# Kernel tuning notes

Hardware: AMD Instinct MI355X
Metric: run time of the kernel (lower is better)

Reference implementation:

```python
import jax, jax.numpy as jnp
from jax import lax
import numpy as np

B, N, C, HEADS = 8, 4096, 512, 16
HD = C // HEADS


def rope2d(x, h, w, base=10000.0):
    # x: [b, h, w, c]; 2D axial RoPE as in the torch `rope` helper
    c = x.shape[-1]
    k_max = c // 4  # feature_dim // (2 * len(channel_dims))
    theta = 1.0 / (base ** (jnp.arange(k_max, dtype=jnp.float32) / k_max))  # [k_max]
    ii = jnp.arange(h, dtype=jnp.float32)[:, None, None]  # row index
    jj = jnp.arange(w, dtype=jnp.float32)[None, :, None]  # col index
    ang = jnp.concatenate([
        jnp.broadcast_to(ii * theta, (h, w, k_max)),
        jnp.broadcast_to(jj * theta, (h, w, k_max)),
    ], axis=-1)  # [h, w, c//2]
    cos, sin = jnp.cos(ang), jnp.sin(ang)
    xp = x.reshape(x.shape[0], h, w, c // 2, 2)
    xr, xi = xp[..., 0], xp[..., 1]
    out = jnp.stack([xr * cos - xi * sin, xi * cos + xr * sin], axis=-1)
    return out.reshape(x.shape)


def setup_inputs() -> dict:
    key = jax.random.key(0)
    k1, k2, k3, k4, k5 = jax.random.split(key, 5)
    x = jax.random.normal(k1, (B, N, C), dtype=jnp.float32)
    Wqk = jax.random.normal(k2, (C, 2 * C), dtype=jnp.float32) * 0.02
    bqk = jax.random.normal(k3, (2 * C,), dtype=jnp.float32) * 0.02
    lepe_w = jax.random.normal(k4, (C, 1, 3, 3), dtype=jnp.float32) * 0.05  # depthwise OIHW
    lepe_b = jax.random.normal(k5, (C,), dtype=jnp.float32) * 0.02
    return {"x": x, "h": 64, "w": 64, "Wqk": Wqk, "bqk": bqk, "lepe_w": lepe_w, "lepe_b": lepe_b}


def reference(x, h, w, Wqk, bqk, lepe_w, lepe_b):
    b, n, c = x.shape
    hd = c // HEADS
    qk = x @ Wqk + bqk                       # [b, n, 2c]
    q = jax.nn.elu(qk[..., :c]) + 1.0        # ELU+1 feature map
    k = jax.nn.elu(qk[..., c:]) + 1.0
    v = x
    q_rope = rope2d(q.reshape(b, h, w, c), h, w).reshape(b, n, HEADS, hd)
    k_rope = rope2d(k.reshape(b, h, w, c), h, w).reshape(b, n, HEADS, hd)
    qh = q.reshape(b, n, HEADS, hd)
    kh = k.reshape(b, n, HEADS, hd)
    vh = v.reshape(b, n, HEADS, hd)
    k_mean = kh.mean(axis=1)                 # [b, HEADS, hd]
    z = 1.0 / (jnp.einsum('bnhd,bhd->bnh', qh, k_mean) + 1e-6)  # [b, n, HEADS]
    inv_n = 1.0 / jnp.float32(n)
    kv = jnp.einsum('bnhd,bnhe->bhde', k_rope, vh) * inv_n       # [b, HEADS, hd, hd]
    attn = jnp.einsum('bnhd,bhde->bnhe', q_rope, kv) * z[..., None]
    out = attn.reshape(b, n, c)
    # depthwise 3x3 LePE on v (== x) as NCHW image
    v_img = x.reshape(b, h, w, c).transpose(0, 3, 1, 2)
    lepe = lax.conv_general_dilated(v_img, lepe_w, (1, 1), 'SAME',
                                    feature_group_count=c,
                                    dimension_numbers=('NCHW', 'OIHW', 'NCHW'))
    lepe = lepe + lepe_b[None, :, None, None]
    out = out + lepe.transpose(0, 2, 3, 1).reshape(b, n, c)
    return out
```

## Files before the change

### kernel.cpp

```cpp
#include <hip/hip_runtime.h>
#include <stdint.h>

static constexpr int BATCH = 8;
static constexpr int NTOK  = 4096;
static constexpr int CDIM  = 512;
static constexpr int NCOL  = 1024;
static constexpr int MROWS = BATCH * NTOK;
static constexpr int KDIM  = 512;

static constexpr size_t OFF_KSUM = 0;
static constexpr size_t OFF_KV   = 16384;
static constexpr size_t OFF_XB   = 540672;
static constexpr size_t OFF_WT   = OFF_XB + 33554432;
static constexpr size_t OFF_QP   = OFF_WT + 1048576;
static constexpr size_t OFF_KR   = OFF_QP + 33554432;
static constexpr size_t OFF_TRIG = OFF_KR + 33554432;
static constexpr size_t OFF_WT9  = OFF_TRIG + 65536;
static constexpr size_t WS_NEED  = OFF_WT9 + 18432;

static constexpr int KV_CHUNKS = 64;
static constexpr int KV_OUT    = BATCH * 16 * 32 * 32;

typedef __attribute__((ext_vector_type(8))) short bf16x8;
typedef __attribute__((ext_vector_type(4))) float f32x4;
typedef __attribute__((ext_vector_type(8))) unsigned short u16x8;

__device__ __forceinline__ float bf2f(unsigned short u) {
  union { unsigned int i; float f; } v; v.i = ((unsigned int)u) << 16; return v.f;
}
__device__ __forceinline__ unsigned short f2bf(float f) {
  union { float f; unsigned int i; } v; v.f = f;
  unsigned int b = v.i + 0x7FFFu + ((v.i >> 16) & 1u);
  return (unsigned short)(b >> 16);
}
__device__ __forceinline__ void gload16(const void* g, void* l) {
  __builtin_amdgcn_global_load_lds(
      (const __attribute__((address_space(1))) unsigned int*)g,
      (__attribute__((address_space(3))) unsigned int*)l,
      16, 0, 0);
}
__device__ __forceinline__ float elu1(float v) {
  return v > 0.f ? v + 1.f : __expf(v);
}

__global__ void prep_kernel(const float* __restrict__ x, const float* __restrict__ Wqk,
                            const float* __restrict__ lepe_w,
                            float* __restrict__ wsf, unsigned short* __restrict__ xb,
                            unsigned short* __restrict__ wT, float2* __restrict__ trig,
                            float* __restrict__ wt9) {
  const int ZN = (int)(OFF_XB / 4);
  const int XN = MROWS * CDIM / 8;
  const int WN = (KDIM * NCOL) / 8;
  const int TN = 64 * 128;
  const int W9 = 9 * 512;
  const int total = ZN + XN + WN + TN + W9;
  for (int i = blockIdx.x * blockDim.x + threadIdx.x; i < total;
       i += gridDim.x * blockDim.x) {
    if (i < ZN) {
      wsf[i] = 0.f;
    } else if (i < ZN + XN) {
      const int j = i - ZN;
      const float4* xp = (const float4*)x + (size_t)j * 2;
      const float4 a = xp[0], b4 = xp[1];
      u16x8 o;
      o[0] = f2bf(a.x);  o[1] = f2bf(a.y);  o[2] = f2bf(a.z);  o[3] = f2bf(a.w);
      o[4] = f2bf(b4.x); o[5] = f2bf(b4.y); o[6] = f2bf(b4.z); o[7] = f2bf(b4.w);
      *((u16x8*)xb + j) = o;
    } else if (i < ZN + XN + WN) {
      const int j = i - ZN - XN;
      const int nc8 = j & 127;
      const int k   = j >> 7;
      const float4* wp = (const float4*)(Wqk + (size_t)k * NCOL + nc8 * 8);
      const float4 a = wp[0], b4 = wp[1];
      const float vals[8] = {a.x, a.y, a.z, a.w, b4.x, b4.y, b4.z, b4.w};
      const int nc0 = nc8 * 8;
#pragma unroll
      for (int t = 0; t < 8; ++t) wT[(size_t)(nc0 + t) * KDIM + k] = f2bf(vals[t]);
    } else if (i < ZN + XN + WN + TN) {
      const int j = i - ZN - XN - WN;
      const int tt = j & 127;
      const int pos = j >> 7;
      const float theta = __expf(-(float)tt * 0.07195578415f);
      const float ang = (float)pos * theta;
      float s, c;
      sincosf(ang, &s, &c);
      trig[pos * 128 + tt] = make_float2(c, s);
    } else {
      const int j = i - ZN - XN - WN - TN;
      const int tap = j >> 9;
      const int c   = j & 511;
      wt9[tap * 512 + c] = lepe_w[c * 9 + tap];
    }
  }
}

__global__ __launch_bounds__(512)
void gemm_kernel(const unsigned short* __restrict__ xb, const unsigned short* __restrict__ wT,
                 const float* __restrict__ bqk, const float2* __restrict__ trig,
                 unsigned short* __restrict__ qp, unsigned short* __restrict__ kr,
                 float* __restrict__ ksum) {
  __shared__ __align__(16) unsigned short S[3][2][8192];
  float* Cst = (float*)&S[0][0][0];
  const int tid = threadIdx.x;
  const int wid = tid >> 6;
  const int l = tid & 63;
  const int la = l & 15, lg = l >> 4;
  const int wm = wid >> 2, wn = wid & 3;
  const int nt = blockIdx.x;
  const int m0 = blockIdx.y * 256;
  const int n0 = nt * 256;

  f32x4 acc[8][4];
#pragma unroll
  for (int i = 0; i < 8; ++i)
#pragma unroll
    for (int j = 0; j < 4; ++j) acc[i][j] = (f32x4){0.f, 0.f, 0.f, 0.f};

  const int srow = tid >> 2;
  const int scol = ((tid & 3) ^ ((tid >> 3) & 3)) * 8;
  const int rsw = (la >> 1) & 3;
  const int rslot = (lg ^ rsw) * 8;

#define STG_A(kt, bb, rr) gload16(xb + (size_t)(m0 + (rr) * 128 + srow) * KDIM + (kt) * 32 + scol, \
                                  &S[bb][0][(rr) * 4096 + tid * 8])
#define STG_B(kt, bb, rr) gload16(wT + (size_t)(n0 + (rr) * 128 + srow) * KDIM + (kt) * 32 + scol, \
                                  &S[bb][1][(rr) * 4096 + tid * 8])

  STG_A(0, 0, 0); STG_A(0, 0, 1); STG_B(0, 0, 0); STG_B(0, 0, 1);
  STG_A(1, 1, 0); STG_A(1, 1, 1); STG_B(1, 1, 0); STG_B(1, 1, 1);
  asm volatile("s_waitcnt vmcnt(4)" ::: "memory");
  __builtin_amdgcn_s_barrier();
  __builtin_amdgcn_sched_barrier(0);

  for (int kt = 0; kt < 16; ++kt) {
    const int cur = kt % 3;
    const int nx2 = (kt + 2) % 3;
    bf16x8 af[4], bf[4];
#pragma unroll
    for (int i = 0; i < 4; ++i)
      af[i] = *(const bf16x8*)&S[cur][0][(wm * 128 + i * 16 + la) * 32 + rslot];
#pragma unroll
    for (int j = 0; j < 4; ++j)
      bf[j] = *(const bf16x8*)&S[cur][1][(wn * 64 + j * 16 + la) * 32 + rslot];
    if (kt + 2 < 16) { STG_A(kt + 2, nx2, 0); STG_A(kt + 2, nx2, 1); }
    __builtin_amdgcn_s_barrier();
    asm volatile("s_waitcnt lgkmcnt(0)" ::: "memory");
    __builtin_amdgcn_sched_barrier(0);
    __builtin_amdgcn_s_setprio(1);
#pragma unroll
    for (int i = 0; i < 4; ++i)
#pragma unroll
      for (int j = 0; j < 4; ++j)
        acc[i][j] = __builtin_amdgcn_mfma_f32_16x16x32_bf16(af[i], bf[j], acc[i][j], 0, 0, 0);
    __builtin_amdgcn_s_setprio(0);
    __builtin_amdgcn_s_barrier();
#pragma unroll
    for (int i = 0; i < 4; ++i)
      af[i] = *(const bf16x8*)&S[cur][0][(wm * 128 + (4 + i) * 16 + la) * 32 + rslot];
    if (kt + 2 < 16) { STG_B(kt + 2, nx2, 0); STG_B(kt + 2, nx2, 1); }
    __builtin_amdgcn_s_barrier();
    asm volatile("s_waitcnt lgkmcnt(0)" ::: "memory");
    __builtin_amdgcn_sched_barrier(0);
    __builtin_amdgcn_s_setprio(1);
#pragma unroll
    for (int i = 0; i < 4; ++i)
#pragma unroll
      for (int j = 0; j < 4; ++j)
        acc[4 + i][j] = __builtin_amdgcn_mfma_f32_16x16x32_bf16(af[i], bf[j], acc[4 + i][j], 0, 0, 0);
    __builtin_amdgcn_s_setprio(0);
    if (kt < 14) {
      asm volatile("s_waitcnt vmcnt(4)" ::: "memory");
    } else if (kt == 14) {
      asm volatile("s_waitcnt vmcnt(0)" ::: "memory");
    }
    __builtin_amdgcn_s_barrier();
    __builtin_amdgcn_sched_barrier(0);
  }
#undef STG_A
#undef STG_B

  const bool isq = (nt < 2);
  const int bidx = m0 >> 12;
  float colsum[4] = {0.f, 0.f, 0.f, 0.f};
#pragma unroll
  for (int j = 0; j < 4; ++j) {
    const float bias = bqk[n0 + wn * 64 + j * 16 + la];
#pragma unroll
    for (int i = 0; i < 8; ++i) {
#pragma unroll
      for (int r = 0; r < 4; ++r) {
        const float v = elu1(acc[i][j][r] + bias);
        acc[i][j][r] = v;
        if (!isq) colsum[j] += v;
      }
    }
  }
  if (!isq) {
#pragma unroll
    for (int j = 0; j < 4; ++j) {
      float s = colsum[j];
      s += __shfl_xor(s, 16);
      s += __shfl_xor(s, 32);
      if (lg == 0) {
        atomicAdd(&ksum[bidx * CDIM + (n0 - 512) + wn * 64 + j * 16 + la], s);
      }
    }
  }

  for (int cc = 0; cc < 8; ++cc) {
    __syncthreads();
    if (wm == (cc >> 2)) {
      const int mi0 = (cc & 3) * 2;
#pragma unroll
      for (int mil = 0; mil < 2; ++mil) {
#pragma unroll
        for (int j = 0; j < 4; ++j) {
#pragma unroll
          for (int r = 0; r < 4; ++r) {
            Cst[(mil * 16 + lg * 4 + r) * 260 + wn * 64 + j * 16 + la] = acc[mi0 + mil][j][r];
          }
        }
      }
    }
    __syncthreads();
#pragma unroll
    for (int it = 0; it < 2; ++it) {
      const int idx = it * 512 + tid;
      const int rowloc = idx >> 5;
      const int seg = idx & 31;
      const int grow = m0 + cc * 32 + rowloc;
      const int lcol = seg * 8;
      float v[8];
      *(float2*)&v[0] = *(const float2*)&Cst[rowloc * 260 + lcol + 0];
      *(float2*)&v[2] = *(const float2*)&Cst[rowloc * 260 + lcol + 2];
      *(float2*)&v[4] = *(const float2*)&Cst[rowloc * 260 + lcol + 4];
      *(float2*)&v[6] = *(const float2*)&Cst[rowloc * 260 + lcol + 6];
      if (isq) {
        u16x8 o;
#pragma unroll
        for (int jj = 0; jj < 8; ++jj) o[jj] = f2bf(v[jj]);
        *(u16x8*)(qp + (size_t)grow * CDIM + n0 + lcol) = o;
      } else {
        const int ck0 = (n0 - 512) + lcol;
        const int n = grow & (NTOK - 1);
        const int p0 = ck0 >> 1;
        const int pos = (p0 >= 128) ? (n & 63) : (n >> 6);
        const float4 t01 = *(const float4*)&trig[pos * 128 + (p0 & 127)];
        const float4 t23 = *(const float4*)&trig[pos * 128 + (p0 & 127) + 2];
        u16x8 o;
        o[0] = f2bf(v[0] * t01.x - v[1] * t01.y);
        o[1] = f2bf(v[1] * t01.x + v[0] * t01.y);
        o[2] = f2bf(v[2] * t01.z - v[3] * t01.w);
        o[3] = f2bf(v[3] * t01.z + v[2] * t01.w);
        o[4] = f2bf(v[4] * t23.x - v[5] * t23.y);
        o[5] = f2bf(v[5] * t23.x + v[4] * t23.y);
        o[6] = f2bf(v[6] * t23.z - v[7] * t23.w);
        o[7] = f2bf(v[7] * t23.z + v[6] * t23.w);
        *(u16x8*)(kr + (size_t)grow * CDIM + ck0) = o;
      }
    }
  }
}

__global__ __launch_bounds__(512)
void kvpart_kernel(const unsigned short* __restrict__ kr, const unsigned short* __restrict__ xb,
                   float* __restrict__ part) {
  const int bid = blockIdx.x;
  const int b = bid >> 6, ch = bid & 63;
  const int t = threadIdx.x;
  const int h = t >> 5;
  const int sub = t & 31;
  const int d0 = (sub >> 2) * 4, e0 = (sub & 3) * 8;

  float acc[4][8];
#pragma unroll
  for (int i = 0; i < 4; ++i)
#pragma unroll
    for (int j = 0; j < 8; ++j) acc[i][j] = 0.f;

  const size_t rowbase = (size_t)(b * NTOK + ch * 64) * CDIM + h * 32;
  ushort4 k4 = *(const ushort4*)(kr + rowbase + d0);
  u16x8 v8 = *(const u16x8*)(xb + rowbase + e0);
#pragma unroll 2
  for (int r = 0; r < 64; ++r) {
    ushort4 kn = k4;
    u16x8 vn = v8;
    if (r < 63) {
      const size_t offn = rowbase + (size_t)(r + 1) * CDIM;
      kn = *(const ushort4*)(kr + offn + d0);
      vn = *(const u16x8*)(xb + offn + e0);
    }
    const float kf0 = bf2f(k4.x), kf1 = bf2f(k4.y), kf2 = bf2f(k4.z), kf3 = bf2f(k4.w);
    float vf[8];
#pragma unroll
    for (int j = 0; j < 8; ++j) vf[j] = bf2f(v8[j]);
#pragma unroll
    for (int j = 0; j < 8; ++j) {
      acc[0][j] += kf0 * vf[j];
      acc[1][j] += kf1 * vf[j];
      acc[2][j] += kf2 * vf[j];
      acc[3][j] += kf3 * vf[j];
    }
    k4 = kn;
    v8 = vn;
  }

  float* p = part + ((size_t)ch * BATCH * 16 + b * 16 + h) * 1024;
#pragma unroll
  for (int i = 0; i < 4; ++i) {
    *(float4*)&p[(d0 + i) * 32 + e0 + 0] = *(float4*)&acc[i][0];
    *(float4*)&p[(d0 + i) * 32 + e0 + 4] = *(float4*)&acc[i][4];
  }
}

__global__ __launch_bounds__(256)
void kvred_kernel(const float* __restrict__ part, float* __restrict__ kv) {
  const int o = blockIdx.x * 256 + threadIdx.x;
  float s0 = 0.f, s1 = 0.f, s2 = 0.f, s3 = 0.f;
#pragma unroll
  for (int ch = 0; ch < KV_CHUNKS; ch += 4) {
    s0 += part[(size_t)(ch + 0) * KV_OUT + o];
    s1 += part[(size_t)(ch + 1) * KV_OUT + o];
    s2 += part[(size_t)(ch + 2) * KV_OUT + o];
    s3 += part[(size_t)(ch + 3) * KV_OUT + o];
  }
  kv[o] = (s0 + s1 + s2 + s3) * (1.0f / (float)NTOK);
}

__global__ __launch_bounds__(256)
void out4_kernel(const unsigned short* __restrict__ qp, const float* __restrict__ ksum,
                 const float* __restrict__ kv, const float2* __restrict__ trig,
                 const unsigned short* __restrict__ xb, const float* __restrict__ wt9,
                 const float* __restrict__ lepe_b, float* __restrict__ out) {
  __shared__ __align__(16) float kvs[32 * 32];
  __shared__ __align__(16) float qrs[32 * 40];
  const int y = blockIdx.x;
  const int h = blockIdx.y >> 1, half = blockIdx.y & 1;
  const int b = blockIdx.z;
  const int t = threadIdx.x;
  const int e8 = t & 7, tok = t >> 3;
  const int c4 = e8 * 4;

  ((float4*)kvs)[t] = ((const float4*)(kv + (size_t)(b * 16 + h) * 1024))[t];

  const float4 ks4 = *(const float4*)(ksum + b * CDIM + h * 32 + c4);
  const float4 lb4 = *(const float4*)(lepe_b + h * 32 + c4);
  float4 w4[9];
#pragma unroll
  for (int tap = 0; tap < 9; ++tap)
    w4[tap] = *(const float4*)(wt9 + tap * CDIM + h * 32 + c4);
  const int pbase = (h * 16 + e8 * 2) & 127;
  __syncthreads();

  const float inv_n = 1.0f / (float)NTOK;
  const int col = half * 32 + tok;
  const int n = y * 64 + col;
  const size_t rowoff = ((size_t)(b * NTOK + n)) * CDIM + h * 32;

  const ushort4 q4u = *(const ushort4*)(qp + rowoff + c4);
  const float q0 = bf2f(q4u.x), q1 = bf2f(q4u.y), q2 = bf2f(q4u.z), q3 = bf2f(q4u.w);
  float zs = q0 * ks4.x + q1 * ks4.y + q2 * ks4.z + q3 * ks4.w;
  zs += __shfl_xor(zs, 1);
  zs += __shfl_xor(zs, 2);
  zs += __shfl_xor(zs, 4);
  const float z = 1.0f / (zs * inv_n + 1e-6f);
  const int pos = (h >= 8) ? col : y;
  const float4 cs01 = *(const float4*)&trig[pos * 128 + pbase];
  float4 qr;
  qr.x = q0 * cs01.x - q1 * cs01.y;
  qr.y = q1 * cs01.x + q0 * cs01.y;
  qr.z = q2 * cs01.z - q3 * cs01.w;
  qr.w = q3 * cs01.z + q2 * cs01.w;
  *(float4*)&qrs[tok * 40 + c4] = qr;
  float4 acc = lb4;
#pragma unroll
  for (int dy = 0; dy < 3; ++dy) {
    const int iy = y + dy - 1;
    if (iy < 0 || iy > 63) continue;
#pragma unroll
    for (int dx = 0; dx < 3; ++dx) {
      const int ix = col + dx - 1;
      if (ix < 0 || ix > 63) continue;
      const ushort4 xv = *(const ushort4*)(xb + ((size_t)(b * NTOK) + iy * 64 + ix) * CDIM + h * 32 + c4);
      const float4 wv = w4[dy * 3 + dx];
      acc.x += bf2f(xv.x) * wv.x; acc.y += bf2f(xv.y) * wv.y;
      acc.z += bf2f(xv.z) * wv.z; acc.w += bf2f(xv.w) * wv.w;
    }
  }
  float4 attn = {0.f, 0.f, 0.f, 0.f};
#pragma unroll
  for (int dg = 0; dg < 8; ++dg) {
    const float4 qv = *(const float4*)&qrs[tok * 40 + dg * 4];
#pragma unroll
    for (int j = 0; j < 4; ++j) {
      const float qs = (j == 0) ? qv.x : (j == 1) ? qv.y : (j == 2) ? qv.z : qv.w;
      const float4 kvr = *(const float4*)&kvs[(dg * 4 + j) * 32 + c4];
      attn.x += qs * kvr.x; attn.y += qs * kvr.y;
      attn.z += qs * kvr.z; attn.w += qs * kvr.w;
    }
  }
  float4 res;
  res.x = attn.x * z + acc.x;
  res.y = attn.y * z + acc.y;
  res.z = attn.z * z + acc.z;
  res.w = attn.w * z + acc.w;
  *(float4*)(out + rowoff + c4) = res;
}

extern "C" void kernel_launch(void* const* d_in, const int* in_sizes, int n_in,
                              void* d_out, int out_size, void* d_ws, size_t ws_size,
                              hipStream_t stream) {
  const float* x      = (const float*)d_in[0];
  const float* Wqk    = (const float*)d_in[3];
  const float* bqk    = (const float*)d_in[4];
  const float* lepe_w = (const float*)d_in[5];
  const float* lepe_b = (const float*)d_in[6];
  float* out = (float*)d_out;

  if (ws_size < WS_NEED) return;

  char* ws = (char*)d_ws;
  float* ksum            = (float*)(ws + OFF_KSUM);
  float* kv              = (float*)(ws + OFF_KV);
  unsigned short* xb     = (unsigned short*)(ws + OFF_XB);
  unsigned short* wT     = (unsigned short*)(ws + OFF_WT);
  unsigned short* qp     = (unsigned short*)(ws + OFF_QP);
  unsigned short* kr     = (unsigned short*)(ws + OFF_KR);
  float2* trig           = (float2*)(ws + OFF_TRIG);
  float* wt9             = (float*)(ws + OFF_WT9);
  float* part            = (float*)d_out;

  hipLaunchKernelGGL(prep_kernel, dim3(2048), dim3(256), 0, stream,
                     x, Wqk, lepe_w, (float*)ws, xb, wT, trig, wt9);
  hipLaunchKernelGGL(gemm_kernel, dim3(4, MROWS / 256), dim3(512), 0, stream,
                     xb, wT, bqk, trig, qp, kr, ksum);
  hipLaunchKernelGGL(kvpart_kernel, dim3(BATCH * KV_CHUNKS), dim3(512), 0, stream,
                     kr, xb, part);
  hipLaunchKernelGGL(kvred_kernel, dim3(KV_OUT / 256), dim3(256), 0, stream,
                     part, kv);
  hipLaunchKernelGGL(out4_kernel, dim3(64, 32, 8), dim3(256), 0, stream,
                     qp, ksum, kv, trig, xb, wt9, lepe_b, out);
}
```

Before: 174.0 us.

## Stage kv partial products through triple-buffered LDS with async global loads

Rewrites the kv partial-product kernel to stream K and V rows into a triple-buffered shared-memory ring using async global-to-LDS loads, overlapping the next tile's load with compute. Each thread now accumulates an 8x8 register tile instead of 4x8, and blocks cover 128 rows with 256 threads, halving the chunk count and the partial buffer the reduction must read. It aims to cut global-load latency stalls and reduction traffic, at the cost of more registers per thread, fewer blocks in flight, and barrier overhead.

```diff
diff --git a/kernel.cpp b/kernel.cpp
--- a/kernel.cpp
+++ b/kernel.cpp
@@ -18,7 +18,7 @@
 static constexpr size_t OFF_WT9  = OFF_TRIG + 65536;
 static constexpr size_t WS_NEED  = OFF_WT9 + 18432;
 
-static constexpr int KV_CHUNKS = 64;
+static constexpr int KV_CHUNKS = 32;
 static constexpr int KV_OUT    = BATCH * 16 * 32 * 32;
 
 typedef __attribute__((ext_vector_type(8))) short bf16x8;
@@ -262,52 +262,63 @@
   }
 }
 
-__global__ __launch_bounds__(512)
+__global__ __launch_bounds__(256)
 void kvpart_kernel(const unsigned short* __restrict__ kr, const unsigned short* __restrict__ xb,
                    float* __restrict__ part) {
+  __shared__ __align__(16) unsigned short kbuf[3][8 * 512];
+  __shared__ __align__(16) unsigned short vbuf[3][8 * 512];
   const int bid = blockIdx.x;
-  const int b = bid >> 6, ch = bid & 63;
+  const int b = bid >> 5, ch = bid & 31;
   const int t = threadIdx.x;
-  const int h = t >> 5;
-  const int sub = t & 31;
-  const int d0 = (sub >> 2) * 4, e0 = (sub & 3) * 8;
-
-  float acc[4][8];
-#pragma unroll
-  for (int i = 0; i < 4; ++i)
+  const int h = t >> 4;
+  const int sub = t & 15;
+  const int d0 = (sub >> 2) * 8, e0 = (sub & 3) * 8;
+  const int srow = t >> 6;
+  const int scol = (t & 63) * 8;
+  const size_t base = (size_t)(b * NTOK + ch * 128) * CDIM;
+
+  float acc[8][8];
+#pragma unroll
+  for (int i = 0; i < 8; ++i)
 #pragma unroll
     for (int j = 0; j < 8; ++j) acc[i][j] = 0.f;
 
-  const size_t rowbase = (size_t)(b * NTOK + ch * 64) * CDIM + h * 32;
-  ushort4 k4 = *(const ushort4*)(kr + rowbase + d0);
-  u16x8 v8 = *(const u16x8*)(xb + rowbase + e0);
-#pragma unroll 2
-  for (int r = 0; r < 64; ++r) {
-    ushort4 kn = k4;
-    u16x8 vn = v8;
-    if (r < 63) {
-      const size_t offn = rowbase + (size_t)(r + 1) * CDIM;
-      kn = *(const ushort4*)(kr + offn + d0);
-      vn = *(const u16x8*)(xb + offn + e0);
-    }
-    const float kf0 = bf2f(k4.x), kf1 = bf2f(k4.y), kf2 = bf2f(k4.z), kf3 = bf2f(k4.w);
-    float vf[8];
-#pragma unroll
-    for (int j = 0; j < 8; ++j) vf[j] = bf2f(v8[j]);
-#pragma unroll
-    for (int j = 0; j < 8; ++j) {
-      acc[0][j] += kf0 * vf[j];
-      acc[1][j] += kf1 * vf[j];
-      acc[2][j] += kf2 * vf[j];
-      acc[3][j] += kf3 * vf[j];
-    }
-    k4 = kn;
-    v8 = vn;
-  }
+#define KVSTG(tt, bb) do {                                                                  \
+    gload16(kr + base + (size_t)((tt) * 8 + srow) * CDIM + scol,     &kbuf[bb][srow * 512 + scol]);       \
+    gload16(kr + base + (size_t)((tt) * 8 + 4 + srow) * CDIM + scol, &kbuf[bb][(4 + srow) * 512 + scol]); \
+    gload16(xb + base + (size_t)((tt) * 8 + srow) * CDIM + scol,     &vbuf[bb][srow * 512 + scol]);       \
+    gload16(xb + base + (size_t)((tt) * 8 + 4 + srow) * CDIM + scol, &vbuf[bb][(4 + srow) * 512 + scol]); \
+  } while (0)
+
+  KVSTG(0, 0);
+  for (int tt = 0; tt < 16; ++tt) {
+    const int cb = tt % 3;
+    if (tt < 15) {
+      KVSTG(tt + 1, (tt + 1) % 3);
+      asm volatile("s_waitcnt vmcnt(4)" ::: "memory");
+    } else {
+      asm volatile("s_waitcnt vmcnt(0)" ::: "memory");
+    }
+    __builtin_amdgcn_s_barrier();
+#pragma unroll
+    for (int r = 0; r < 8; ++r) {
+      const u16x8 k8 = *(const u16x8*)&kbuf[cb][r * 512 + h * 32 + d0];
+      const u16x8 v8 = *(const u16x8*)&vbuf[cb][r * 512 + h * 32 + e0];
+      float kf[8], vf[8];
+#pragma unroll
+      for (int i = 0; i < 8; ++i) { kf[i] = bf2f(k8[i]); vf[i] = bf2f(v8[i]); }
+#pragma unroll
+      for (int i = 0; i < 8; ++i)
+#pragma unroll
+        for (int j = 0; j < 8; ++j) acc[i][j] += kf[i] * vf[j];
+    }
+    __builtin_amdgcn_s_barrier();
+  }
+#undef KVSTG
 
   float* p = part + ((size_t)ch * BATCH * 16 + b * 16 + h) * 1024;
 #pragma unroll
-  for (int i = 0; i < 4; ++i) {
+  for (int i = 0; i < 8; ++i) {
     *(float4*)&p[(d0 + i) * 32 + e0 + 0] = *(float4*)&acc[i][0];
     *(float4*)&p[(d0 + i) * 32 + e0 + 4] = *(float4*)&acc[i][4];
   }
@@ -434,7 +445,7 @@
                      x, Wqk, lepe_w, (float*)ws, xb, wT, trig, wt9);
   hipLaunchKernelGGL(gemm_kernel, dim3(4, MROWS / 256), dim3(512), 0, stream,
                      xb, wT, bqk, trig, qp, kr, ksum);
-  hipLaunchKernelGGL(kvpart_kernel, dim3(BATCH * KV_CHUNKS), dim3(512), 0, stream,
+  hipLaunchKernelGGL(kvpart_kernel, dim3(BATCH * KV_CHUNKS), dim3(256), 0, stream,
                      kr, xb, part);
   hipLaunchKernelGGL(kvred_kernel, dim3(KV_OUT / 256), dim3(256), 0, stream,
                      part, kv);
```

Result: faster. 166.5 us (-4.3%).
